# Performance work log

Measured on AMD Instinct MI355X. Metric: run time of the kernel, lower is better.

## Reference

```python
import jax, jax.numpy as jnp
import numpy as np


COMMITMENT_COST = 0.25


def setup_inputs() -> dict:
    key = jax.random.key(0)
    k1, k2 = jax.random.split(key)
    B, C, H, W = 16, 128, 64, 64
    K = 1024
    z = jax.random.normal(k1, (B, C, H, W), dtype=jnp.float32)
    # original init: uniform(-1/K, 1/K); keep that scale for faithfulness
    codebook = jax.random.uniform(k2, (K, C), dtype=jnp.float32,
                                  minval=-1.0 / K, maxval=1.0 / K)
    return {"z": z, "codebook": codebook}


def reference(z, codebook):
    B, C, H, W = z.shape
    K = codebook.shape[0]
    # (B,C,H,W) -> (N,C) with N = B*H*W
    z_flat = jnp.transpose(z, (0, 2, 3, 1)).reshape(-1, C)
    # squared-distance matrix (N,K): ||z||^2 + ||e||^2 - 2 z.e
    dists = (jnp.sum(z_flat ** 2, axis=1, keepdims=True)
             + jnp.sum(codebook ** 2, axis=1)
             - 2.0 * z_flat @ codebook.T)
    indices = jnp.argmin(dists, axis=1)  # (N,)
    z_q = jnp.transpose(codebook[indices].reshape(B, H, W, C), (0, 3, 1, 2))
    commitment_loss = jnp.mean((jax.lax.stop_gradient(z_q) - z) ** 2)
    codebook_loss = jnp.mean((z_q - jax.lax.stop_gradient(z)) ** 2)
    vq_loss = codebook_loss + COMMITMENT_COST * commitment_loss
    # straight-through estimator
    z_q_st = z + jax.lax.stop_gradient(z_q - z)
    usage = jnp.sum(jnp.bincount(indices, length=K) > 0).astype(jnp.float32) / K
    return (z_q_st, vq_loss, usage)
```

## Files before the change

### kernel.cpp

```cpp
#include <hip/hip_runtime.h>

typedef __attribute__((ext_vector_type(8))) short short8;
typedef __attribute__((ext_vector_type(4))) float f32x4;

#define C_DIM 128
#define K_CODES 1024
#define TOT 8388608
#define NBLK 512

__device__ __forceinline__ unsigned int f2bf1(float f) {
  unsigned int u = __float_as_uint(f);
  return (u + 0x7FFFu + ((u >> 16) & 1u)) >> 16;
}
__device__ __forceinline__ unsigned int f2bf2(float lo, float hi) {
  return f2bf1(lo) | (f2bf1(hi) << 16);
}

union U16x8 { uint4 u; short8 s; };

__global__ void prep_kernel(const float* __restrict__ cb,
                            unsigned short* __restrict__ ebf,
                            float* __restrict__ nsq1,
                            int* __restrict__ used) {
  int gid = blockIdx.x * 256 + threadIdx.x;
  ebf[gid] = (unsigned short)f2bf1(cb[gid]);
  if (gid < K_CODES) {
    float s = 0.f;
    #pragma unroll 8
    for (int c = 0; c < C_DIM; ++c) { float v = cb[gid * C_DIM + c]; s += v * v; }
    nsq1[gid] = 1.0f + s;
    used[gid] = 0;
  }
}

__global__ __launch_bounds__(256, 4)
void vq_main(const float* __restrict__ zin, const float* __restrict__ cb,
             const unsigned short* __restrict__ ebf,
             const float* __restrict__ nsq1,
             int* __restrict__ used, float* __restrict__ lossp,
             float* __restrict__ out) {
  __shared__ __align__(16) uint4 bG[2][1024];
  __shared__ float nsq_s[K_CODES];
  __shared__ int   widx[128];
  __shared__ float wsum[4];

  const int t  = threadIdx.x;
  const int L  = t & 63;
  const int wv = t >> 6;
  const int q  = L >> 4;
  const int nL = L & 15;

  const int bb = blockIdx.x >> 5;
  const int hg = blockIdx.x & 31;
  const int zoff = bb * (C_DIM * 4096) + hg * 128;

  for (int i = t; i < K_CODES; i += 256) nsq_s[i] = nsq1[i];

  short8 afrag[8];
  #pragma unroll
  for (int mt = 0; mt < 2; ++mt) {
    const int wcol = wv * 32 + mt * 16 + nL;
    #pragma unroll
    for (int ks = 0; ks < 4; ++ks) {
      float v[8];
      #pragma unroll
      for (int u = 0; u < 8; ++u)
        v[u] = zin[zoff + (ks * 32 + q * 8 + u) * 4096 + wcol];
      U16x8 pk;
      pk.u.x = f2bf2(-2.f * v[0], -2.f * v[1]);
      pk.u.y = f2bf2(-2.f * v[2], -2.f * v[3]);
      pk.u.z = f2bf2(-2.f * v[4], -2.f * v[5]);
      pk.u.w = f2bf2(-2.f * v[6], -2.f * v[7]);
      afrag[mt * 4 + ks] = pk.s;
    }
  }

  const uint4* __restrict__ ebv = (const uint4*)ebf;
  const int nLw = t >> 4;
  const int oct = t & 15;
  const int sks = oct >> 2, sq = oct & 3;

  #pragma unroll
  for (int p = 0; p < 4; ++p) {
    int r = p * 16 + nLw;
    bG[0][p * 256 + sks * 64 + nLw * 4 + sq] = ebv[r * 16 + oct];
  }
  __syncthreads();

  unsigned int kmin[8];
  #pragma unroll
  for (int i = 0; i < 8; ++i) kmin[i] = 0xFFFFFFFFu;

  #pragma unroll 1
  for (int ch = 0; ch < 16; ++ch) {
    const int cur = ch & 1;
    if (ch < 15) {
      #pragma unroll
      for (int p = 0; p < 4; ++p) {
        int r = p * 16 + nLw;
        bG[cur ^ 1][p * 256 + sks * 64 + nLw * 4 + sq] =
            ebv[((ch + 1) * 64 + r) * 16 + oct];
      }
    }
    const short8* bp = (const short8*)bG[cur];
    #pragma unroll
    for (int jj = 0; jj < 4; ++jj) {
      const int row = ch * 64 + jj * 16 + nL;
      short8 b0 = bp[jj * 256 + 0 * 64 + nL * 4 + q];
      short8 b1 = bp[jj * 256 + 1 * 64 + nL * 4 + q];
      short8 b2 = bp[jj * 256 + 2 * 64 + nL * 4 + q];
      short8 b3 = bp[jj * 256 + 3 * 64 + nL * 4 + q];
      const float nv = nsq_s[row];
      f32x4 a0 = {nv, nv, nv, nv};
      f32x4 a1 = {nv, nv, nv, nv};
      a0 = __builtin_amdgcn_mfma_f32_16x16x32_bf16(afrag[0], b0, a0, 0, 0, 0);
      a1 = __builtin_amdgcn_mfma_f32_16x16x32_bf16(afrag[4], b0, a1, 0, 0, 0);
      a0 = __builtin_amdgcn_mfma_f32_16x16x32_bf16(afrag[1], b1, a0, 0, 0, 0);
      a1 = __builtin_amdgcn_mfma_f32_16x16x32_bf16(afrag[5], b1, a1, 0, 0, 0);
      a0 = __builtin_amdgcn_mfma_f32_16x16x32_bf16(afrag[2], b2, a0, 0, 0, 0);
      a1 = __builtin_amdgcn_mfma_f32_16x16x32_bf16(afrag[6], b2, a1, 0, 0, 0);
      a0 = __builtin_amdgcn_mfma_f32_16x16x32_bf16(afrag[3], b3, a0, 0, 0, 0);
      a1 = __builtin_amdgcn_mfma_f32_16x16x32_bf16(afrag[7], b3, a1, 0, 0, 0);
      const unsigned int rowc = (unsigned int)row;
      #pragma unroll
      for (int r = 0; r < 4; ++r) {
        unsigned int k0 = (__float_as_uint(a0[r]) & 0xFFFFFC00u) | rowc;
        if (k0 < kmin[r]) kmin[r] = k0;
        unsigned int k1 = (__float_as_uint(a1[r]) & 0xFFFFFC00u) | rowc;
        if (k1 < kmin[4 + r]) kmin[4 + r] = k1;
      }
    }
    __syncthreads();
  }

  #pragma unroll
  for (int m = 1; m <= 8; m <<= 1) {
    #pragma unroll
    for (int i = 0; i < 8; ++i) {
      unsigned int o = (unsigned int)__shfl_xor((int)kmin[i], m, 64);
      if (o < kmin[i]) kmin[i] = o;
    }
  }
  if (nL == 0) {
    #pragma unroll
    for (int mt = 0; mt < 2; ++mt)
      #pragma unroll
      for (int r = 0; r < 4; ++r) {
        int bi = (int)(kmin[mt * 4 + r] & 1023u);
        widx[wv * 32 + mt * 16 + q * 4 + r] = bi;
        used[bi] = 1;
      }
  }
  __syncthreads();

  float lsum = 0.f;
  {
    const int p = t & 127, cg = t >> 7;
    const int idx = widx[p];
    const uint4* erow = ebv + idx * 16 + cg * 8;
    const int obase = zoff + cg * 64 * 4096 + p;
    #pragma unroll 2
    for (int i = 0; i < 8; ++i) {
      uint4 g = erow[i];
      const unsigned int wrd[4] = {g.x, g.y, g.z, g.w};
      #pragma unroll
      for (int half = 0; half < 4; ++half) {
        float e0 = __uint_as_float(wrd[half] << 16);
        float e1 = __uint_as_float(wrd[half] & 0xFFFF0000u);
        int off = obase + (i * 8 + half * 2) * 4096;
        float d0 = zin[off] - e0;
        out[off] = e0;
        lsum += d0 * d0;
        off += 4096;
        float d1 = zin[off] - e1;
        out[off] = e1;
        lsum += d1 * d1;
      }
    }
  }
  #pragma unroll
  for (int o = 32; o > 0; o >>= 1) lsum += __shfl_down(lsum, o, 64);
  if (L == 0) wsum[wv] = lsum;
  __syncthreads();
  if (t == 0) lossp[blockIdx.x] = wsum[0] + wsum[1] + wsum[2] + wsum[3];
}

__global__ void finalize_kernel(const int* __restrict__ used,
                                const float* __restrict__ lossp,
                                float* __restrict__ out2) {
  __shared__ int   redi[256];
  __shared__ float redf[256];
  int t = threadIdx.x;
  int s = 0;
  for (int i = t; i < K_CODES; i += 256) s += (used[i] != 0) ? 1 : 0;
  float ls = 0.f;
  for (int i = t; i < NBLK; i += 256) ls += lossp[i];
  redi[t] = s; redf[t] = ls;
  __syncthreads();
  for (int o = 128; o > 0; o >>= 1) {
    if (t < o) { redi[t] += redi[t + o]; redf[t] += redf[t + o]; }
    __syncthreads();
  }
  if (t == 0) {
    out2[0] = 1.25f * redf[0] / (float)TOT;
    out2[1] = (float)redi[0] / 1024.0f;
  }
}

extern "C" void kernel_launch(void* const* d_in, const int* in_sizes, int n_in,
                              void* d_out, int out_size, void* d_ws, size_t ws_size,
                              hipStream_t stream) {
  const float* z  = (const float*)d_in[0];
  const float* cb = (const float*)d_in[1];
  float* out = (float*)d_out;
  char* ws = (char*)d_ws;
  unsigned short* ebf = (unsigned short*)ws;
  float* nsq1  = (float*)(ws + 262144);
  int*   used  = (int*)(ws + 266240);
  float* lossp = (float*)(ws + 270336);

  hipLaunchKernelGGL(prep_kernel, dim3(512), dim3(256), 0, stream,
                     cb, ebf, nsq1, used);
  hipLaunchKernelGGL(vq_main, dim3(NBLK), dim3(256), 0, stream,
                     z, cb, ebf, nsq1, used, lossp, out);
  hipLaunchKernelGGL(finalize_kernel, dim3(1), dim3(256), 0, stream,
                     used, lossp, out + TOT);
}
```

Measured before the change: 119.5 us.

## Split codebook across wave pairs with 64-column A tiles per wave

Each wave now holds A fragments for 64 spatial columns instead of 32, and the wave pairs split each codebook chunk's 64 rows in half. Each B fragment loaded from LDS is therefore reused across four MFMA tiles instead of two, which roughly halves LDS reads per MFMA. Each pair's partial argmin is merged through shared memory with an extra barrier. In exchange, register pressure roughly doubles for afrag and kmin, and the launch bound is lowered from 4 to 3 blocks per SM, so occupancy may drop.

```diff
diff --git a/kernel.cpp b/kernel.cpp
--- a/kernel.cpp
+++ b/kernel.cpp
@@ -33,7 +33,7 @@
   }
 }
 
-__global__ __launch_bounds__(256, 4)
+__global__ __launch_bounds__(256, 3)
 void vq_main(const float* __restrict__ zin, const float* __restrict__ cb,
              const unsigned short* __restrict__ ebf,
              const float* __restrict__ nsq1,
@@ -41,12 +41,15 @@
              float* __restrict__ out) {
   __shared__ __align__(16) uint4 bG[2][1024];
   __shared__ float nsq_s[K_CODES];
+  __shared__ unsigned int mergeK[128][2];
   __shared__ int   widx[128];
   __shared__ float wsum[4];
 
   const int t  = threadIdx.x;
   const int L  = t & 63;
   const int wv = t >> 6;
+  const int ph = wv >> 1;
+  const int kh = wv & 1;
   const int q  = L >> 4;
   const int nL = L & 15;
 
@@ -56,10 +59,10 @@
 
   for (int i = t; i < K_CODES; i += 256) nsq_s[i] = nsq1[i];
 
-  short8 afrag[8];
-  #pragma unroll
-  for (int mt = 0; mt < 2; ++mt) {
-    const int wcol = wv * 32 + mt * 16 + nL;
+  short8 afrag[16];
+  #pragma unroll
+  for (int mt = 0; mt < 4; ++mt) {
+    const int wcol = ph * 64 + mt * 16 + nL;
     #pragma unroll
     for (int ks = 0; ks < 4; ++ks) {
       float v[8];
@@ -87,9 +90,9 @@
   }
   __syncthreads();
 
-  unsigned int kmin[8];
-  #pragma unroll
-  for (int i = 0; i < 8; ++i) kmin[i] = 0xFFFFFFFFu;
+  unsigned int kmin[16];
+  #pragma unroll
+  for (int i = 0; i < 16; ++i) kmin[i] = 0xFFFFFFFFu;
 
   #pragma unroll 1
   for (int ch = 0; ch < 16; ++ch) {
@@ -104,7 +107,8 @@
     }
     const short8* bp = (const short8*)bG[cur];
     #pragma unroll
-    for (int jj = 0; jj < 4; ++jj) {
+    for (int j2 = 0; j2 < 2; ++j2) {
+      const int jj = kh * 2 + j2;
       const int row = ch * 64 + jj * 16 + nL;
       short8 b0 = bp[jj * 256 + 0 * 64 + nL * 4 + q];
       short8 b1 = bp[jj * 256 + 1 * 64 + nL * 4 + q];
@@ -113,14 +117,24 @@
       const float nv = nsq_s[row];
       f32x4 a0 = {nv, nv, nv, nv};
       f32x4 a1 = {nv, nv, nv, nv};
-      a0 = __builtin_amdgcn_mfma_f32_16x16x32_bf16(afrag[0], b0, a0, 0, 0, 0);
-      a1 = __builtin_amdgcn_mfma_f32_16x16x32_bf16(afrag[4], b0, a1, 0, 0, 0);
-      a0 = __builtin_amdgcn_mfma_f32_16x16x32_bf16(afrag[1], b1, a0, 0, 0, 0);
-      a1 = __builtin_amdgcn_mfma_f32_16x16x32_bf16(afrag[5], b1, a1, 0, 0, 0);
-      a0 = __builtin_amdgcn_mfma_f32_16x16x32_bf16(afrag[2], b2, a0, 0, 0, 0);
-      a1 = __builtin_amdgcn_mfma_f32_16x16x32_bf16(afrag[6], b2, a1, 0, 0, 0);
-      a0 = __builtin_amdgcn_mfma_f32_16x16x32_bf16(afrag[3], b3, a0, 0, 0, 0);
-      a1 = __builtin_amdgcn_mfma_f32_16x16x32_bf16(afrag[7], b3, a1, 0, 0, 0);
+      f32x4 a2 = {nv, nv, nv, nv};
+      f32x4 a3 = {nv, nv, nv, nv};
+      a0 = __builtin_amdgcn_mfma_f32_16x16x32_bf16(afrag[0],  b0, a0, 0, 0, 0);
+      a1 = __builtin_amdgcn_mfma_f32_16x16x32_bf16(afrag[4],  b0, a1, 0, 0, 0);
+      a2 = __builtin_amdgcn_mfma_f32_16x16x32_bf16(afrag[8],  b0, a2, 0, 0, 0);
+      a3 = __builtin_amdgcn_mfma_f32_16x16x32_bf16(afrag[12], b0, a3, 0, 0, 0);
+      a0 = __builtin_amdgcn_mfma_f32_16x16x32_bf16(afrag[1],  b1, a0, 0, 0, 0);
+      a1 = __builtin_amdgcn_mfma_f32_16x16x32_bf16(afrag[5],  b1, a1, 0, 0, 0);
+      a2 = __builtin_amdgcn_mfma_f32_16x16x32_bf16(afrag[9],  b1, a2, 0, 0, 0);
+      a3 = __builtin_amdgcn_mfma_f32_16x16x32_bf16(afrag[13], b1, a3, 0, 0, 0);
+      a0 = __builtin_amdgcn_mfma_f32_16x16x32_bf16(afrag[2],  b2, a0, 0, 0, 0);
+      a1 = __builtin_amdgcn_mfma_f32_16x16x32_bf16(afrag[6],  b2, a1, 0, 0, 0);
+      a2 = __builtin_amdgcn_mfma_f32_16x16x32_bf16(afrag[10], b2, a2, 0, 0, 0);
+      a3 = __builtin_amdgcn_mfma_f32_16x16x32_bf16(afrag[14], b2, a3, 0, 0, 0);
+      a0 = __builtin_amdgcn_mfma_f32_16x16x32_bf16(afrag[3],  b3, a0, 0, 0, 0);
+      a1 = __builtin_amdgcn_mfma_f32_16x16x32_bf16(afrag[7],  b3, a1, 0, 0, 0);
+      a2 = __builtin_amdgcn_mfma_f32_16x16x32_bf16(afrag[11], b3, a2, 0, 0, 0);
+      a3 = __builtin_amdgcn_mfma_f32_16x16x32_bf16(afrag[15], b3, a3, 0, 0, 0);
       const unsigned int rowc = (unsigned int)row;
       #pragma unroll
       for (int r = 0; r < 4; ++r) {
@@ -128,6 +142,10 @@
         if (k0 < kmin[r]) kmin[r] = k0;
         unsigned int k1 = (__float_as_uint(a1[r]) & 0xFFFFFC00u) | rowc;
         if (k1 < kmin[4 + r]) kmin[4 + r] = k1;
+        unsigned int k2 = (__float_as_uint(a2[r]) & 0xFFFFFC00u) | rowc;
+        if (k2 < kmin[8 + r]) kmin[8 + r] = k2;
+        unsigned int k3 = (__float_as_uint(a3[r]) & 0xFFFFFC00u) | rowc;
+        if (k3 < kmin[12 + r]) kmin[12 + r] = k3;
       }
     }
     __syncthreads();
@@ -136,20 +154,25 @@
   #pragma unroll
   for (int m = 1; m <= 8; m <<= 1) {
     #pragma unroll
-    for (int i = 0; i < 8; ++i) {
+    for (int i = 0; i < 16; ++i) {
       unsigned int o = (unsigned int)__shfl_xor((int)kmin[i], m, 64);
       if (o < kmin[i]) kmin[i] = o;
     }
   }
   if (nL == 0) {
     #pragma unroll
-    for (int mt = 0; mt < 2; ++mt)
-      #pragma unroll
-      for (int r = 0; r < 4; ++r) {
-        int bi = (int)(kmin[mt * 4 + r] & 1023u);
-        widx[wv * 32 + mt * 16 + q * 4 + r] = bi;
-        used[bi] = 1;
-      }
+    for (int mt = 0; mt < 4; ++mt)
+      #pragma unroll
+      for (int r = 0; r < 4; ++r)
+        mergeK[ph * 64 + mt * 16 + q * 4 + r][kh] = kmin[mt * 4 + r];
+  }
+  __syncthreads();
+
+  if (t < 128) {
+    unsigned int b = min(mergeK[t][0], mergeK[t][1]);
+    int bi = (int)(b & 1023u);
+    widx[t] = bi;
+    used[bi] = 1;
   }
   __syncthreads();
 
```

Measured after the change: 117.5 us. No clear change (-1.7%).
